# Kernel tuning notes

Measured on AMD Instinct MI355X. Metric: run time of the kernel, lower is better.

## Reference

```python
import jax, jax.numpy as jnp
import numpy as np

# ---- dimensions ----
N_MOL, N_PER = 256, 32
N = N_MOL * N_PER                      # 8192 nodes
E = N_MOL * N_PER * (N_PER - 1)        # 253952 fully-connected directed edges
SDIM, VDIM, EDIM = 256, 64, 32
NAF, NBT, LAT = 16, 5, 64
LAYERS = 5
MSG_IN = 2 * SDIM + EDIM + 2           # [s_i, s_j, e, d, a]
MSG_OUT = SDIM + VDIM + 1 + EDIM       # scalar msg, vec weights, pos weight, edge update
BOND_IN = SDIM + EDIM + 1
BOND_HID = 128


def _block_fc_edges():
    # fully-connected (no self loops) edges within each molecule of N_PER atoms
    idx = np.arange(N_PER)
    src, tgt = np.meshgrid(idx, idx, indexing='ij')
    mask = src != tgt
    src, tgt = src[mask], tgt[mask]
    offs = (np.arange(N_MOL) * N_PER)[:, None]
    S = (src[None, :] + offs).reshape(-1)
    T = (tgt[None, :] + offs).reshape(-1)
    return np.stack([S, T], 0).astype(np.int64)


def setup_inputs() -> dict:
    key = jax.random.key(0)
    ks = jax.random.split(key, 16)
    edge_index = jnp.asarray(_block_fc_edges())
    batch = jnp.asarray(np.repeat(np.arange(N_MOL), N_PER).astype(np.int64))
    return dict(
        x=jax.random.normal(ks[0], (N, NAF), jnp.float32),
        z=jax.random.normal(ks[1], (N, LAT), jnp.float32),
        rot=jax.random.normal(ks[2], (N_MOL, 3, 3), jnp.float32),
        edge_index_global=edge_index,
        edge_attr_global=jax.random.normal(ks[3], (E, NBT), jnp.float32),
        batch=batch,
        # atom/bond input mappings (DenseLayer == Linear)
        Wam=jax.random.normal(ks[4], (NAF + LAT, SDIM + 3), jnp.float32) * 0.05,
        bam=jnp.zeros((SDIM + 3,), jnp.float32),
        Wbm=jax.random.normal(ks[5], (NBT, EDIM), jnp.float32) * 0.3,
        bbm=jnp.zeros((EDIM,), jnp.float32),
        # stacked per-layer EQGAT message-MLP weights
        gW1=jax.random.normal(ks[6], (LAYERS, MSG_IN, SDIM), jnp.float32) * 0.03,
        gb1=jnp.zeros((LAYERS, SDIM), jnp.float32),
        gW2=jax.random.normal(ks[7], (LAYERS, SDIM, MSG_OUT), jnp.float32) * 0.05,
        gb2=jnp.zeros((LAYERS, MSG_OUT), jnp.float32),
        # prediction heads
        Wh1=jax.random.normal(ks[8], (SDIM, SDIM), jnp.float32) * 0.05,
        bh1=jnp.zeros((SDIM,), jnp.float32),
        Wh2=jax.random.normal(ks[9], (SDIM, NAF), jnp.float32) * 0.05,
        bh2=jnp.zeros((NAF,), jnp.float32),
        We1=jax.random.normal(ks[10], (BOND_IN, BOND_HID), jnp.float32) * 0.05,
        be1=jnp.zeros((BOND_HID,), jnp.float32),
        We2=jax.random.normal(ks[11], (BOND_HID, NBT), jnp.float32) * 0.05,
        be2=jnp.zeros((NBT,), jnp.float32),
    )


def _edge_attrs(pos, src, tgt):
    # faithful to Decoder.calculate_edge_attrs (sqrt=True)
    r = pos[tgt] - pos[src]                       # [E,3]
    a = jnp.sum(pos[tgt] * pos[src], -1)          # [E]
    d = jnp.sqrt(jnp.clip(jnp.sum(r * r, -1), 1e-6))
    r_norm = r / (1.0 + d)[:, None]
    return d, a, r_norm


def reference(x, z, rot, edge_index_global, edge_attr_global, batch,
              Wam, bam, Wbm, bbm, gW1, gb1, gW2, gb2,
              Wh1, bh1, Wh2, bh2, We1, be1, We2, be2):
    src, tgt = edge_index_global[0], edge_index_global[1]
    n = x.shape[0]
    # atom mapping + split into scalar feats and positions
    h = jnp.concatenate([x, z], -1) @ Wam + bam
    s, pos = h[:, :SDIM], h[:, SDIM:]
    # per-graph rotation of positions
    pos = jnp.einsum('bij,bj->bi', rot[batch], pos)
    # bond mapping
    e = edge_attr_global @ Wbm + bbm
    v = jnp.zeros((n, 3, VDIM), x.dtype)
    # segment-mean denominator (in-degree), fixed since edge_index is fixed
    cnt = jnp.clip(jax.ops.segment_sum(jnp.ones((src.shape[0],), x.dtype), tgt,
                                       num_segments=n), 1.0)

    def seg_mean(m):
        out = jax.ops.segment_sum(m, tgt, num_segments=n)
        return out / cnt.reshape((n,) + (1,) * (m.ndim - 1))

    def layer(carry, p):
        s, v, pos, e = carry
        W1, b1, W2, b2 = p
        d, a, r_norm = _edge_attrs(pos, src, tgt)   # recompute_edge_attributes=True
        feat = jnp.concatenate([s[src], s[tgt], e, d[:, None], a[:, None]], -1)
        hdn = jax.nn.silu(feat @ W1 + b1)
        m = hdn @ W2 + b2
        m_s = m[:, :SDIM]
        m_v = m[:, SDIM:SDIM + VDIM]
        m_p = m[:, SDIM + VDIM:SDIM + VDIM + 1]
        m_e = m[:, SDIM + VDIM + 1:]
        s = s + seg_mean(m_s)                                   # scalar update
        v = v + seg_mean(r_norm[:, :, None] * m_v[:, None, :])  # equivariant vec update
        pos = pos + seg_mean(r_norm * m_p)                      # equivariant pos update
        e = e + m_e                                             # edge feature update
        return (s, v, pos, e), None

    (s, v, pos, e), _ = jax.lax.scan(layer, (s, v, pos, e), (gW1, gb1, gW2, gb2))

    # prediction head: atom logits, bond logits (symmetric s_i+s_j), coords
    atoms = jax.nn.silu(s @ Wh1 + bh1) @ Wh2 + bh2
    d, a, r_norm = _edge_attrs(pos, src, tgt)
    ef = jnp.concatenate([s[src] + s[tgt], e, d[:, None]], -1)
    bonds = jax.nn.silu(ef @ We1 + be1) @ We2 + be2
    return atoms, bonds, pos
```

## Files before the change

kernel.cpp:

```cpp
#include <hip/hip_runtime.h>
#include <hip/hip_bf16.h>
#include <cstdint>
#include <cstddef>

#define N_MOLS 256
#define NN     8192
#define SDIM_  256
#define NAF_   16
#define LAYERS_ 5

typedef __attribute__((ext_vector_type(8)))  short bf16x8;
typedef __attribute__((ext_vector_type(16))) float f32x16;
typedef __attribute__((ext_vector_type(4)))  float f32x4;

__device__ __forceinline__ float silu_f(float x) {
    return x * __builtin_amdgcn_rcpf(1.f + __expf(-x));
}
__device__ __forceinline__ short bfc(float f) {
    __hip_bfloat16 h = __float2bfloat16(f);
    return __builtin_bit_cast(short, h);
}
__device__ __forceinline__ float bf2f(short h) {
    union { uint32_t u; float f; } v; v.u = ((uint32_t)(unsigned short)h) << 16; return v.f;
}
#define ONEBF ((short)0x3F80)

#define OFF_T1    0
#define OFF_W2ST  655360
#define OFF_WH1T  983040
#define OFF_WE1T  1048576
#define OFF_W1CG  1081344
#define OFF_W1DA  1122304
#define OFF_W2P   1124864
#define OFF_W2EI  1126144
#define OFF_WE1CG 1167104
#define OFF_WD    1171200
#define OFF_WE2I  1171328
#define OFF_WH2T  1175424
#define W_TOTAL   1179520

__global__ __launch_bounds__(256) void init_all(
    const float* __restrict__ x, const float* __restrict__ z,
    const float* __restrict__ rot, const float* __restrict__ Wam,
    const float* __restrict__ bam, const float* __restrict__ ea,
    const float* __restrict__ Wbm, const float* __restrict__ bbm,
    const float* __restrict__ gW1, const float* __restrict__ gW2,
    const float* __restrict__ Wh1, const float* __restrict__ We1,
    const float* __restrict__ We2, const float* __restrict__ Wh2,
    float* __restrict__ s, short* __restrict__ sbf, float* __restrict__ pos,
    short* __restrict__ ebuf, short* __restrict__ wb)
{
    __shared__ __align__(16) char smem[20608];
    const int b = blockIdx.x, t = threadIdx.x;
    if (b < 1024) {
        for (int o = b * 256 + t; o < W_TOTAL; o += 1024 * 256) {
            float v;
            if (o < OFF_W2ST) {
                const int l = o >> 17, r = o & 131071;
                const int j2 = r >> 8, k = r & 255;
                v = gW1[(size_t)l * 139776 + (size_t)((j2 >> 8) * 256 + k) * 256 + (j2 & 255)];
            } else if (o < OFF_WH1T) {
                const int q = o - OFF_W2ST;
                const int l = q >> 16, r = q & 65535;
                const int n = r >> 8, k = r & 255;
                v = gW2[(size_t)l * 90368 + (size_t)k * 353 + n];
            } else if (o < OFF_WE1T) {
                const int q = o - OFF_WH1T;
                v = Wh1[(size_t)(q & 255) * 256 + (q >> 8)];
            } else if (o < OFF_W1CG) {
                const int q = o - OFF_WE1T;
                v = We1[(size_t)(q & 255) * 128 + (q >> 8)];
            } else if (o < OFF_W1DA) {
                const int q = o - OFF_W1CG;
                const int l = q >> 13, r = q & 8191;
                const int j = r >> 5, w = r & 31;
                v = gW1[(size_t)l * 139776 + (size_t)(512 + w) * 256 + j];
            } else if (o < OFF_W2P) {
                const int q = o - OFF_W1DA;
                const int l = q >> 9, r = q & 511;
                v = gW1[(size_t)l * 139776 + (size_t)(544 + (r >> 8)) * 256 + (r & 255)];
            } else if (o < OFF_W2EI) {
                const int q = o - OFF_W2P;
                v = gW2[(size_t)(q >> 8) * 90368 + (size_t)(q & 255) * 353 + 320];
            } else if (o < OFF_WE1CG) {
                const int q = o - OFF_W2EI;
                const int l = q >> 13, r = q & 8191;
                const int kk = r >> 9, lanei = (r >> 3) & 63, jj = r & 7;
                const int j = kk * 16 + (lanei >> 5) * 8 + jj;
                v = gW2[(size_t)l * 90368 + (size_t)j * 353 + 321 + (lanei & 31)];
            } else if (o < OFF_WD) {
                const int q = o - OFF_WE1CG;
                v = We1[(size_t)(256 + (q & 31)) * 128 + (q >> 5)];
            } else if (o < OFF_WE2I) {
                v = We1[288 * 128 + (o - OFF_WD)];
            } else if (o < OFF_WH2T) {
                const int q = o - OFF_WE2I;
                const int kk = q >> 9, lanei = (q >> 3) & 63, jj = q & 7;
                const int c = lanei & 31;
                v = (c < 5) ? We2[(size_t)(kk * 16 + (lanei >> 5) * 8 + jj) * 5 + c] : 0.f;
            } else {
                const int q = o - OFF_WH2T;
                v = Wh2[(size_t)(q & 255) * 16 + (q >> 8)];
            }
            wb[o] = bfc(v);
        }
    } else if (b < 1280) {
        const int mol = b - 1024;
        float (*xz)[80]  = (float(*)[80])smem;
        float (*praw)[3] = (float(*)[3])(smem + 32 * 80 * 4);
        for (int idx = t; idx < 32 * 80; idx += 256) {
            const int i = idx / 80, k = idx % 80;
            xz[i][k] = (k < 16) ? x[(size_t)(mol * 32 + i) * 16 + k]
                                : z[(size_t)(mol * 32 + i) * 64 + (k - 16)];
        }
        __syncthreads();
        float acc[32];
        #pragma unroll
        for (int i = 0; i < 32; ++i) acc[i] = 0.f;
        for (int k0 = 0; k0 < 80; k0 += 4) {
            const float w0 = Wam[(k0 + 0) * 259 + t];
            const float w1 = Wam[(k0 + 1) * 259 + t];
            const float w2 = Wam[(k0 + 2) * 259 + t];
            const float w3 = Wam[(k0 + 3) * 259 + t];
            #pragma unroll
            for (int i = 0; i < 32; ++i) {
                const float4 xv = *(const float4*)&xz[i][k0];
                acc[i] += xv.x * w0 + xv.y * w1 + xv.z * w2 + xv.w * w3;
            }
        }
        const float bv = bam[t];
        #pragma unroll
        for (int i = 0; i < 32; ++i) {
            const float v = acc[i] + bv;
            s[(size_t)(mol * 32 + i) * 256 + t] = v;
            sbf[(size_t)(mol * 32 + i) * 256 + t] = bfc(v);
        }
        if (t < 96) {
            const int i = t / 3, c = t % 3;
            float a2 = bam[256 + c];
            for (int k = 0; k < 80; ++k) a2 += xz[i][k] * Wam[k * 259 + 256 + c];
            praw[i][c] = a2;
        }
        __syncthreads();
        if (t < 96) {
            const int i = t / 3, c = t % 3;
            float p = 0.f;
            for (int jj = 0; jj < 3; ++jj) p += rot[mol * 9 + c * 3 + jj] * praw[i][jj];
            pos[(size_t)(mol * 32 + i) * 3 + c] = p;
        }
    } else {
        const int mol = b - 1280;
        float* sEa      = (float*)smem;
        float (*sW)[32] = (float(*)[32])(smem + 4960 * 4);
        float* sB       = (float*)(smem + (4960 + 160) * 4);
        const float* base = ea + (size_t)mol * 4960;
        for (int i = t; i < 4960; i += 256) sEa[i] = base[i];
        if (t < 160) sW[t / 32][t & 31] = Wbm[t];
        if (t < 32)  sB[t] = bbm[t];
        __syncthreads();
        for (int i = t; i < 31744; i += 256) {
            const int c = i & 31;
            const int rrn = i >> 5;
            const int n = rrn / 31, rr = rrn - n * 31;
            const int s_ = rr + (rr >= n ? 1 : 0);
            const int gl = s_ * 31 + (n - (n > s_ ? 1 : 0));
            float acc = sB[c];
            #pragma unroll
            for (int k = 0; k < 5; ++k) acc += sEa[gl * 5 + k] * sW[k][c];
            ebuf[(size_t)mol * 31744 + i] = bfc(acc);
        }
    }
}

__global__ __launch_bounds__(512) void edge_mfma(
    const short* __restrict__ sbfA, const short* __restrict__ T1,
    const float* __restrict__ posIn, float* __restrict__ posOut,
    short* __restrict__ ebuf,
    const short* __restrict__ W1cG, const short* __restrict__ W1daP,
    const short* __restrict__ W2pP, const short* __restrict__ W2eimg,
    const short* __restrict__ W2sT,
    const float* __restrict__ b1, const float* __restrict__ b2,
    float* __restrict__ s, short* __restrict__ sbfOut)
{
    const int blk = blockIdx.x;
    const int mol = blk >> 1;
    const int nbase = (blk & 1) * 16;
    const int t = threadIdx.x;
    const int wave = t >> 6, lane = t & 63;
    const int l = lane & 31, half = lane >> 5;
    const int node0 = mol * 32;

    __shared__ __align__(16) short sBg[256][72];
    __shared__ __align__(16) short sM[8][32][40];
    __shared__ __align__(16) short sHrows[16][264];
    __shared__ __align__(16) short sSB[16][264];
    __shared__ float sPosS[32][4];
    __shared__ __align__(16) short sW1da[2][256];
    __shared__ __align__(16) short sW2p[256];
    __shared__ float sP[8][32];
    __shared__ float sPd[16][4];
    short* sSbf = &sM[0][0][0];

    {
        const int j = t & 255, gh = t >> 8;
        const bf16x8 v0 = *(const bf16x8*)&W1cG[j * 32 + gh * 16];
        const bf16x8 v1 = *(const bf16x8*)&W1cG[j * 32 + gh * 16 + 8];
        const int c3 = (j >> 3) & 3;
        const int s0 = ((gh * 2 + 0) + 3 * c3) & 7;
        const int s1 = ((gh * 2 + 1) + 3 * c3) & 7;
        *(bf16x8*)&sBg[j][s0 * 8] = v0;
        *(bf16x8*)&sBg[j][s1 * 8] = v1;
    }
    {
        const int row = t >> 4, ch = (t & 15) * 16;
        const short* src = sbfA + (size_t)(node0 + row) * 256 + ch;
        *(bf16x8*)&sSbf[row * 264 + ch]     = *(const bf16x8*)(src);
        *(bf16x8*)&sSbf[row * 264 + ch + 8] = *(const bf16x8*)(src + 8);
    }
    if (t < 64) {
        short* d = &sW1da[0][0];
        *(bf16x8*)&d[t * 8] = *(const bf16x8*)&W1daP[t * 8];
    }
    if (t < 32) *(bf16x8*)&sW2p[t * 8] = *(const bf16x8*)&W2pP[t * 8];
    if (t < 96) sPosS[t / 3][t % 3] = posIn[node0 * 3 + t];
    __syncthreads();

    {
        const int jt = wave;
        const int j = jt * 32 + l;
        f32x16 accA = {}, accB = {};
        #pragma unroll
        for (int k0 = 0; k0 < 256; k0 += 16) {
            const bf16x8 afr = *(const bf16x8*)&sSbf[l * 264 + k0 + half * 8];
            const bf16x8 bA  = *(const bf16x8*)(T1 + (size_t)(j) * 256 + k0 + half * 8);
            const bf16x8 bB  = *(const bf16x8*)(T1 + (size_t)(256 + j) * 256 + k0 + half * 8);
            accA = __builtin_amdgcn_mfma_f32_32x32x16_bf16(afr, bA, accA, 0,0,0);
            accB = __builtin_amdgcn_mfma_f32_32x32x16_bf16(afr, bB, accB, 0,0,0);
        }
        const int c3 = (j >> 3) & 3;
        #pragma unroll
        for (int r = 0; r < 16; ++r) {
            const int node = (r & 3) + 8 * (r >> 2) + 4 * half;
            const int k = 32 + node;
            const int slot = ((k >> 3) + 3 * c3) & 7;
            sBg[j][slot * 8 + (k & 7)] = bfc(accA[r]);
            const int nl = node - nbase;
            if ((unsigned)nl < 16u) sSB[nl][j] = bfc(accB[r]);
        }
    }
    __syncthreads();

    float b1v[8];
    short w1dv[8], w1av[8];
    #pragma unroll
    for (int cb = 0; cb < 8; ++cb) {
        b1v[cb]  = b1[cb * 32 + l];
        w1dv[cb] = sW1da[0][cb * 32 + l];
        w1av[cb] = sW1da[1][cb * 32 + l];
    }
    const float b2e = b2[321 + l];
    const float b2p = b2[320];
    int bslot[4];
    #pragma unroll
    for (int ks = 0; ks < 4; ++ks)
        bslot[ks] = ((ks * 2 + half) + 3 * ((l >> 3) & 3)) & 7;

    bf16x8 efr0[2], efr1[2];
    #pragma unroll
    for (int ni = 0; ni < 2; ++ni) {
        const int n = nbase + wave + ni * 8;
        const short* ebase = ebuf + ((size_t)((mol * 32 + n) * 31 + l)) * 32;
        efr0[ni] = *(const bf16x8*)(ebase + half * 8);
        efr1[ni] = *(const bf16x8*)(ebase + 16 + half * 8);
    }

    #pragma unroll
    for (int ni = 0; ni < 2; ++ni) {
        const int n = nbase + wave + ni * 8;
        const int nloc = wave + ni * 8;
        const int rrc = (l < 31) ? l : 30;
        const int src = rrc + (rrc >= n ? 1 : 0);
        const float ax = sPosS[n][0],  ay = sPosS[n][1],  az = sPosS[n][2];
        const float bx = sPosS[src][0], by = sPosS[src][1], bz = sPosS[src][2];
        const float rx = ax - bx, ry = ay - by, rz = az - bz;
        const float av = ax * bx + ay * by + az * bz;
        const float dd = sqrtf(fmaxf(rx * rx + ry * ry + rz * rz, 1e-6f));
        const float inv = __builtin_amdgcn_rcpf(1.f + dd);
        const float rnx = rx * inv, rny = ry * inv, rnz = rz * inv;

        const bf16x8 fr0 = efr0[ni];
        const bf16x8 fr1 = efr1[ni];
        bf16x8 fr2 = {}, fr3, fr4;
        if (half == 0) { fr2[0] = bfc(dd); fr2[1] = bfc(av); }
        #pragma unroll
        for (int jj = 0; jj < 8; ++jj) {
            fr3[jj] = (half * 8 + jj == src)      ? ONEBF : (short)0;
            fr4[jj] = (16 + half * 8 + jj == src) ? ONEBF : (short)0;
        }

        const short* W2ei = W2eimg;
        asm volatile("" : "+s"(W2ei));

        f32x16 accC = {}, accP = {};
        float Hacc[8];

        const int g = l >> 3, jlow = l & 7;
        #pragma unroll
        for (int cb = 0; cb < 8; ++cb) {
            const bf16x8 w2e0 = *(const bf16x8*)&W2ei[(size_t)((cb * 2 + 0) * 64 + lane) * 8];
            const bf16x8 w2e1 = *(const bf16x8*)&W2ei[(size_t)((cb * 2 + 1) * 64 + lane) * 8];
            const float sbv = bf2f(sSB[nloc][cb * 32 + l]) + b1v[cb];
            f32x16 acc;
            #pragma unroll
            for (int r = 0; r < 16; ++r) acc[r] = sbv;
            {
                const short* brow = &sBg[cb * 32 + l][0];
                __builtin_amdgcn_s_setprio(1);
                acc = __builtin_amdgcn_mfma_f32_32x32x16_bf16(fr0, *(const bf16x8*)(brow + bslot[0]*8), acc, 0,0,0);
                acc = __builtin_amdgcn_mfma_f32_32x32x16_bf16(fr1, *(const bf16x8*)(brow + bslot[1]*8), acc, 0,0,0);
                acc = __builtin_amdgcn_mfma_f32_32x32x16_bf16(fr3, *(const bf16x8*)(brow + bslot[2]*8), acc, 0,0,0);
                acc = __builtin_amdgcn_mfma_f32_32x32x16_bf16(fr4, *(const bf16x8*)(brow + bslot[3]*8), acc, 0,0,0);
                bf16x8 frB2 = {};
                if (half == 0) { frB2[0] = w1dv[cb]; frB2[1] = w1av[cb]; }
                acc = __builtin_amdgcn_mfma_f32_32x32x16_bf16(fr2, frB2, acc, 0,0,0);
                __builtin_amdgcn_s_setprio(0);
            }
            float hs = 0.f;
            #pragma unroll
            for (int r = 0; r < 16; ++r) {
                const int e = (r & 3) + 8 * (r >> 2) + 4 * half;
                float h = silu_f(acc[r]);
                if (half == 1 && r == 15) h = 0.f;
                hs += h;
                sM[wave][e][((g + (e >> 3)) & 3) * 8 + jlow] = bfc(h);
            }
            Hacc[cb] = hs;
            #pragma unroll
            for (int q = 0; q < 2; ++q) {
                const bf16x8 afr  = *(const bf16x8*)&sM[wave][l][((q * 2 + half + (l >> 3)) & 3) * 8];
                const bf16x8 wpfr = *(const bf16x8*)&sW2p[cb * 32 + q * 16 + half * 8];
                accC = __builtin_amdgcn_mfma_f32_32x32x16_bf16(afr, q ? w2e1 : w2e0, accC, 0,0,0);
                accP = __builtin_amdgcn_mfma_f32_32x32x16_bf16(afr, wpfr, accP, 0,0,0);
            }
        }
        #pragma unroll
        for (int cb = 0; cb < 8; ++cb) {
            const float v = Hacc[cb] + __shfl_xor(Hacc[cb], 32, 64);
            if (lane < 32) sHrows[nloc][cb * 32 + lane] = bfc(v);
        }
        if (l == 0) {
            #pragma unroll
            for (int q4 = 0; q4 < 4; ++q4) {
                float4 pv = { accP[q4 * 4 + 0], accP[q4 * 4 + 1],
                              accP[q4 * 4 + 2], accP[q4 * 4 + 3] };
                *(float4*)&sP[wave][q4 * 8 + 4 * half] = pv;
            }
        }
        const float pown = sP[wave][l];
        const float pfull = (half == 0 && l < 31) ? (pown + b2p) : 0.f;
        float pd0 = rnx * pfull, pd1 = rny * pfull, pd2 = rnz * pfull;
        #pragma unroll
        for (int m = 1; m <= 32; m <<= 1) {
            pd0 += __shfl_xor(pd0, m, 64);
            pd1 += __shfl_xor(pd1, m, 64);
            pd2 += __shfl_xor(pd2, m, 64);
        }
        if (lane == 0) {
            sPd[nloc][0] = pd0;
            sPd[nloc][1] = pd1;
            sPd[nloc][2] = pd2;
        }
        #pragma unroll
        for (int r = 0; r < 16; ++r) {
            const int e = (r & 3) + 8 * (r >> 2) + 4 * half;
            if (e < 31) {
                short* ep = ebuf + ((size_t)((mol * 32 + n) * 31 + e)) * 32 + l;
                *ep = bfc(bf2f(*ep) + accC[r] + b2e);
            }
        }
    }

    __syncthreads();

    {
        const int jb0 = wave * 32;
        const int arow = lane & 15, kg = lane >> 4;
        f32x4 accS0 = {}, accS1 = {};
        #pragma unroll
        for (int k0 = 0; k0 < 256; k0 += 32) {
            const bf16x8 afr = *(const bf16x8*)&sHrows[arow][k0 + kg * 8];
            const bf16x8 bf0 = *(const bf16x8*)&W2sT[(size_t)(jb0 + arow) * 256 + k0 + kg * 8];
            const bf16x8 bf1 = *(const bf16x8*)&W2sT[(size_t)(jb0 + 16 + arow) * 256 + k0 + kg * 8];
            accS0 = __builtin_amdgcn_mfma_f32_16x16x32_bf16(afr, bf0, accS0, 0,0,0);
            accS1 = __builtin_amdgcn_mfma_f32_16x16x32_bf16(afr, bf1, accS1, 0,0,0);
        }
        const int col = lane & 15;
        const int orow = (lane >> 4) * 4;
        const float bv0 = b2[jb0 + col];
        const float bv1 = b2[jb0 + 16 + col];
        #pragma unroll
        for (int r = 0; r < 4; ++r) {
            const int node = node0 + nbase + orow + r;
            {
                float* sp = s + (size_t)node * 256 + jb0 + col;
                const float nv = *sp + accS0[r] * (1.f / 31.f) + bv0;
                *sp = nv;
                sbfOut[(size_t)node * 256 + jb0 + col] = bfc(nv);
            }
            {
                float* sp = s + (size_t)node * 256 + jb0 + 16 + col;
                const float nv = *sp + accS1[r] * (1.f / 31.f) + bv1;
                *sp = nv;
                sbfOut[(size_t)node * 256 + jb0 + 16 + col] = bfc(nv);
            }
        }
    }
    if (t < 48) {
        const int nl = t / 3, c = t % 3;
        const int node = node0 + nbase + nl;
        posOut[(size_t)node * 3 + c] = posIn[(size_t)node * 3 + c] + sPd[nl][c] * (1.f / 31.f);
    }
}

__global__ __launch_bounds__(512) void bond_mfma(
    const short* __restrict__ sbfA, const short* __restrict__ We1T,
    const float* __restrict__ pos, short* __restrict__ ebuf,
    const short* __restrict__ We1cG, const short* __restrict__ WdP,
    const short* __restrict__ We2img, const short* __restrict__ Wh1T,
    const short* __restrict__ Wh2I,
    const float* __restrict__ be1, const float* __restrict__ be2,
    const float* __restrict__ bh1, const float* __restrict__ bh2,
    float* __restrict__ outA, float* __restrict__ outB,
    float* __restrict__ outPos)
{
    const int blk = blockIdx.x;
    const int mol = blk >> 1;
    const int nbase = (blk & 1) * 16;
    const int t = threadIdx.x;
    const int wave = t >> 6, lane = t & 63;
    const int l = lane & 31, half = lane >> 5;
    const int node0 = mol * 32;

    __shared__ __align__(16) short sBg2[128][72];
    __shared__ __align__(16) short sHdnB[8][32][40];
    __shared__ __align__(16) short sU[32][136];
    __shared__ float sPosS[32][4];
    __shared__ __align__(16) short sWd[128];
    short* sSbf = &sHdnB[0][0][0];

    {
        const int j = t & 127, g = t >> 7;
        const bf16x8 v = *(const bf16x8*)&We1cG[j * 32 + g * 8];
        const int slot = (g + 3 * ((j >> 3) & 3)) & 7;
        *(bf16x8*)&sBg2[j][slot * 8] = v;
    }
    {
        const int row = t >> 4, ch = (t & 15) * 16;
        const short* src = sbfA + (size_t)(node0 + row) * 256 + ch;
        *(bf16x8*)&sSbf[row * 264 + ch]     = *(const bf16x8*)(src);
        *(bf16x8*)&sSbf[row * 264 + ch + 8] = *(const bf16x8*)(src + 8);
    }
    if (t < 16) *(bf16x8*)&sWd[t * 8] = *(const bf16x8*)&WdP[t * 8];
    if (t < 96) sPosS[t / 3][t % 3] = pos[node0 * 3 + t];
    __syncthreads();

    if (wave < 4) {
        const int j = wave * 32 + l;
        f32x16 accU = {};
        #pragma unroll
        for (int k0 = 0; k0 < 256; k0 += 16) {
            const bf16x8 afr = *(const bf16x8*)&sSbf[l * 264 + k0 + half * 8];
            const bf16x8 bU  = *(const bf16x8*)(We1T + (size_t)j * 256 + k0 + half * 8);
            accU = __builtin_amdgcn_mfma_f32_32x32x16_bf16(afr, bU, accU, 0,0,0);
        }
        const int c3 = (j >> 3) & 3;
        #pragma unroll
        for (int r = 0; r < 16; ++r) {
            const int node = (r & 3) + 8 * (r >> 2) + 4 * half;
            const short uv = bfc(accU[r]);
            const int k = 32 + node;
            const int slot = ((k >> 3) + 3 * c3) & 7;
            sBg2[j][slot * 8 + (k & 7)] = uv;
            sU[node][j] = uv;
        }
    }

    float be1v[4];
    #pragma unroll
    for (int cb = 0; cb < 4; ++cb) be1v[cb] = be1[cb * 32 + l];
    const float be2v = (l < 5) ? be2[l] : 0.f;
    int bslot[4];
    #pragma unroll
    for (int ks = 0; ks < 4; ++ks)
        bslot[ks] = ((ks * 2 + half) + 3 * ((l >> 3) & 3)) & 7;
    __syncthreads();

    bf16x8 efr0[2], efr1[2];
    #pragma unroll
    for (int ni = 0; ni < 2; ++ni) {
        const int n = nbase + wave + ni * 8;
        const short* ebase = ebuf + ((size_t)((mol * 32 + n) * 31 + l)) * 32;
        efr0[ni] = *(const bf16x8*)(ebase + half * 8);
        efr1[ni] = *(const bf16x8*)(ebase + 16 + half * 8);
    }

    #pragma unroll
    for (int ni = 0; ni < 2; ++ni) {
        const int n = nbase + wave + ni * 8;
        const int rrc = (l < 31) ? l : 30;
        const int src = rrc + (rrc >= n ? 1 : 0);
        const float rx = sPosS[n][0] - sPosS[src][0];
        const float ry = sPosS[n][1] - sPosS[src][1];
        const float rz = sPosS[n][2] - sPosS[src][2];
        const float dd = sqrtf(fmaxf(rx * rx + ry * ry + rz * rz, 1e-6f));

        const bf16x8 fr0 = efr0[ni];
        const bf16x8 fr1 = efr1[ni];
        bf16x8 fr2 = {}, fr3, fr4;
        if (half == 0) fr2[0] = bfc(dd);
        #pragma unroll
        for (int jj = 0; jj < 8; ++jj) {
            fr3[jj] = (half * 8 + jj == src)      ? ONEBF : (short)0;
            fr4[jj] = (16 + half * 8 + jj == src) ? ONEBF : (short)0;
        }

        const short* We2i = We2img;
        asm volatile("" : "+s"(We2i));

        f32x16 accC = {};
        const int g = l >> 3, jlow = l & 7;
        #pragma unroll
        for (int cb = 0; cb < 4; ++cb) {
            const bf16x8 w2f0 = *(const bf16x8*)&We2i[(size_t)((cb * 2 + 0) * 64 + lane) * 8];
            const bf16x8 w2f1 = *(const bf16x8*)&We2i[(size_t)((cb * 2 + 1) * 64 + lane) * 8];
            const float uin = bf2f(sU[n][cb * 32 + l]) + be1v[cb];
            f32x16 acc;
            #pragma unroll
            for (int r = 0; r < 16; ++r) acc[r] = uin;
            {
                const short* brow = &sBg2[cb * 32 + l][0];
                acc = __builtin_amdgcn_mfma_f32_32x32x16_bf16(fr0, *(const bf16x8*)(brow + bslot[0]*8), acc, 0,0,0);
                acc = __builtin_amdgcn_mfma_f32_32x32x16_bf16(fr1, *(const bf16x8*)(brow + bslot[1]*8), acc, 0,0,0);
                acc = __builtin_amdgcn_mfma_f32_32x32x16_bf16(fr3, *(const bf16x8*)(brow + bslot[2]*8), acc, 0,0,0);
                acc = __builtin_amdgcn_mfma_f32_32x32x16_bf16(fr4, *(const bf16x8*)(brow + bslot[3]*8), acc, 0,0,0);
                bf16x8 frWd = {};
                if (half == 0) frWd[0] = sWd[cb * 32 + l];
                acc = __builtin_amdgcn_mfma_f32_32x32x16_bf16(fr2, frWd, acc, 0,0,0);
            }
            #pragma unroll
            for (int r = 0; r < 16; ++r) {
                const int e = (r & 3) + 8 * (r >> 2) + 4 * half;
                sHdnB[wave][e][((g + (e >> 3)) & 3) * 8 + jlow] = bfc(silu_f(acc[r]));
            }
            #pragma unroll
            for (int q = 0; q < 2; ++q) {
                const bf16x8 afr = *(const bf16x8*)&sHdnB[wave][l][((q * 2 + half + (l >> 3)) & 3) * 8];
                accC = __builtin_amdgcn_mfma_f32_32x32x16_bf16(afr, q ? w2f1 : w2f0, accC, 0,0,0);
            }
        }
        if (l < 5) {
            #pragma unroll
            for (int r = 0; r < 16; ++r) {
                const int e = (r & 3) + 8 * (r >> 2) + 4 * half;
                if (e < 31) {
                    const int s_ = e + (e >= n ? 1 : 0);
                    const int ge = (mol * 32 + s_) * 31 + (n - (n > s_ ? 1 : 0));
                    outB[(size_t)ge * 5 + l] = accC[r] + be2v;
                }
            }
        }
    }
    if (t < 48) {
        const int nl = t / 3, c = t % 3;
        const int node = node0 + nbase + nl;
        outPos[(size_t)node * 3 + c] = pos[(size_t)node * 3 + c];
    }

    __syncthreads();
    {
        short* sA3 = &sU[0][0];
        const int row = t >> 5, ch = (t & 31) * 8;
        *(bf16x8*)&sA3[row * 264 + ch] =
            *(const bf16x8*)(sbfA + (size_t)(node0 + nbase + row) * 256 + ch);
    }
    __syncthreads();
    {
        short* sA3 = &sU[0][0];
        short* sT  = &sBg2[0][0];
        const int jb0 = wave * 32;
        const int arow = lane & 15, kg = lane >> 4;
        f32x4 a0 = {}, a1 = {};
        #pragma unroll
        for (int k0 = 0; k0 < 256; k0 += 32) {
            const bf16x8 afr = *(const bf16x8*)&sA3[arow * 264 + k0 + kg * 8];
            const bf16x8 bw0 = *(const bf16x8*)(Wh1T + (size_t)(jb0 + arow) * 256 + k0 + kg * 8);
            const bf16x8 bw1 = *(const bf16x8*)(Wh1T + (size_t)(jb0 + 16 + arow) * 256 + k0 + kg * 8);
            a0 = __builtin_amdgcn_mfma_f32_16x16x32_bf16(afr, bw0, a0, 0,0,0);
            a1 = __builtin_amdgcn_mfma_f32_16x16x32_bf16(afr, bw1, a1, 0,0,0);
        }
        const int col = lane & 15, orow = (lane >> 4) * 4;
        const float bva = bh1[jb0 + col], bvb = bh1[jb0 + 16 + col];
        #pragma unroll
        for (int r = 0; r < 4; ++r) {
            sT[(orow + r) * 264 + jb0 + col]      = bfc(silu_f(a0[r] + bva));
            sT[(orow + r) * 264 + jb0 + 16 + col] = bfc(silu_f(a1[r] + bvb));
        }
    }
    __syncthreads();
    if (wave == 0) {
        short* sT = &sBg2[0][0];
        const int arow = lane & 15, kg = lane >> 4;
        f32x4 a2 = {};
        #pragma unroll
        for (int k0 = 0; k0 < 256; k0 += 32) {
            const bf16x8 afr = *(const bf16x8*)&sT[arow * 264 + k0 + kg * 8];
            const bf16x8 bfr = *(const bf16x8*)(Wh2I + (size_t)arow * 256 + k0 + kg * 8);
            a2 = __builtin_amdgcn_mfma_f32_16x16x32_bf16(afr, bfr, a2, 0,0,0);
        }
        const int col = lane & 15, orow = (lane >> 4) * 4;
        const float bv = bh2[col];
        #pragma unroll
        for (int r = 0; r < 4; ++r)
            outA[(size_t)(node0 + nbase + orow + r) * 16 + col] = a2[r] + bv;
    }
}

extern "C" void kernel_launch(void* const* d_in, const int* in_sizes, int n_in,
                              void* d_out, int out_size, void* d_ws, size_t ws_size,
                              hipStream_t stream) {
    const float* x   = (const float*)d_in[0];
    const float* z   = (const float*)d_in[1];
    const float* rot = (const float*)d_in[2];
    const float* ea  = (const float*)d_in[4];
    const float* Wam = (const float*)d_in[6];
    const float* bam = (const float*)d_in[7];
    const float* Wbm = (const float*)d_in[8];
    const float* bbm = (const float*)d_in[9];
    const float* gW1 = (const float*)d_in[10];
    const float* gb1 = (const float*)d_in[11];
    const float* gW2 = (const float*)d_in[12];
    const float* gb2 = (const float*)d_in[13];
    const float* Wh1 = (const float*)d_in[14];
    const float* bh1 = (const float*)d_in[15];
    const float* Wh2 = (const float*)d_in[16];
    const float* bh2 = (const float*)d_in[17];
    const float* We1 = (const float*)d_in[18];
    const float* be1 = (const float*)d_in[19];
    const float* We2 = (const float*)d_in[20];
    const float* be2 = (const float*)d_in[21];
    float* out = (float*)d_out;

    float* ws  = (float*)d_ws;
    float* s    = ws;
    float* pos  = ws + 2097152;
    short* e    = (short*)(ws + 2121728);
    short* wb   = (short*)(ws + 6184960);
    short* sbf0 = (short*)(ws + 6774784);
    short* sbf1 = (short*)(ws + 10248192);
    float* pos2 = ws + 16539648;

    init_all<<<1536, 256, 0, stream>>>(x, z, rot, Wam, bam, ea, Wbm, bbm,
        gW1, gW2, Wh1, We1, We2, Wh2, s, sbf0, pos, e, wb);

    float* pbuf[2] = { pos, pos2 };
    short* sbb[2] = { sbf0, sbf1 };
    for (int l = 0; l < LAYERS_; ++l) {
        const float* b1 = gb1 + l * 256;
        const float* b2 = gb2 + l * 353;
        edge_mfma<<<2 * N_MOLS, 512, 0, stream>>>(
            sbb[l & 1], wb + OFF_T1 + (size_t)l * 131072,
            pbuf[l & 1], pbuf[(l + 1) & 1], e,
            wb + OFF_W1CG + l * 8192, wb + OFF_W1DA + l * 512,
            wb + OFF_W2P + l * 256, wb + OFF_W2EI + l * 8192,
            wb + OFF_W2ST + (size_t)l * 65536,
            b1, b2, s, sbb[(l + 1) & 1]);
    }
    float* posF = pbuf[LAYERS_ & 1];
    short* sbfF = sbb[LAYERS_ & 1];

    bond_mfma<<<2 * N_MOLS, 512, 0, stream>>>(
        sbfF, wb + OFF_WE1T, posF, e, wb + OFF_WE1CG, wb + OFF_WD,
        wb + OFF_WE2I, wb + OFF_WH1T, wb + OFF_WH2T,
        be1, be2, bh1, bh2, out, out + 131072, out + 131072 + 1269760);
}
```

Measured before the change: 581.8 us.

## Fuse all five message-passing layers into one persistent per-molecule kernel

Replaces the five per-layer edge kernel launches (two blocks per molecule) with a single 1024-thread block per molecule that loops over layers. Node scalar bf16 features and positions stay in shared memory across layers, which removes the global round-trips, the ping-pong buffers and the launch gaps between layers. It also stops the duplicated T1 GEMM: previously each half-block recomputed both halves, now the 16 waves split the work. The cost is one block per molecule, so only 256 blocks, more shared memory per block and possibly lower occupancy.

```diff
diff --git a/kernel.cpp b/kernel.cpp
--- a/kernel.cpp
+++ b/kernel.cpp
@@ -172,253 +172,268 @@
     }
 }
 
-__global__ __launch_bounds__(512) void edge_mfma(
-    const short* __restrict__ sbfA, const short* __restrict__ T1,
-    const float* __restrict__ posIn, float* __restrict__ posOut,
-    short* __restrict__ ebuf,
-    const short* __restrict__ W1cG, const short* __restrict__ W1daP,
-    const short* __restrict__ W2pP, const short* __restrict__ W2eimg,
-    const short* __restrict__ W2sT,
-    const float* __restrict__ b1, const float* __restrict__ b2,
-    float* __restrict__ s, short* __restrict__ sbfOut)
+__global__ __launch_bounds__(1024) void mol_layers(
+    short* __restrict__ sbf_g, float* __restrict__ pos_g,
+    short* __restrict__ ebuf, const short* __restrict__ wb,
+    const float* __restrict__ gb1, const float* __restrict__ gb2,
+    float* __restrict__ s)
 {
-    const int blk = blockIdx.x;
-    const int mol = blk >> 1;
-    const int nbase = (blk & 1) * 16;
+    const int mol = blockIdx.x;
     const int t = threadIdx.x;
-    const int wave = t >> 6, lane = t & 63;
+    const int w = t >> 6, lane = t & 63;
     const int l = lane & 31, half = lane >> 5;
+    const int vw = w & 7, vb = w >> 3;
+    const int nbase = vb * 16;
     const int node0 = mol * 32;
 
     __shared__ __align__(16) short sBg[256][72];
-    __shared__ __align__(16) short sM[8][32][40];
-    __shared__ __align__(16) short sHrows[16][264];
-    __shared__ __align__(16) short sSB[16][264];
+    __shared__ __align__(16) short sM[16][32][40];
+    __shared__ __align__(16) short sHrows[32][264];
+    __shared__ __align__(16) short sSB[32][264];
+    __shared__ __align__(16) short sSbfP[32][264];
     __shared__ float sPosS[32][4];
     __shared__ __align__(16) short sW1da[2][256];
     __shared__ __align__(16) short sW2p[256];
-    __shared__ float sP[8][32];
-    __shared__ float sPd[16][4];
-    short* sSbf = &sM[0][0][0];
+    __shared__ float sP[16][32];
+    __shared__ float sPd[32][4];
 
     {
-        const int j = t & 255, gh = t >> 8;
-        const bf16x8 v0 = *(const bf16x8*)&W1cG[j * 32 + gh * 16];
-        const bf16x8 v1 = *(const bf16x8*)&W1cG[j * 32 + gh * 16 + 8];
-        const int c3 = (j >> 3) & 3;
-        const int s0 = ((gh * 2 + 0) + 3 * c3) & 7;
-        const int s1 = ((gh * 2 + 1) + 3 * c3) & 7;
-        *(bf16x8*)&sBg[j][s0 * 8] = v0;
-        *(bf16x8*)&sBg[j][s1 * 8] = v1;
-    }
-    {
-        const int row = t >> 4, ch = (t & 15) * 16;
-        const short* src = sbfA + (size_t)(node0 + row) * 256 + ch;
-        *(bf16x8*)&sSbf[row * 264 + ch]     = *(const bf16x8*)(src);
-        *(bf16x8*)&sSbf[row * 264 + ch + 8] = *(const bf16x8*)(src + 8);
-    }
-    if (t < 64) {
-        short* d = &sW1da[0][0];
-        *(bf16x8*)&d[t * 8] = *(const bf16x8*)&W1daP[t * 8];
-    }
-    if (t < 32) *(bf16x8*)&sW2p[t * 8] = *(const bf16x8*)&W2pP[t * 8];
-    if (t < 96) sPosS[t / 3][t % 3] = posIn[node0 * 3 + t];
-    __syncthreads();
-
-    {
-        const int jt = wave;
-        const int j = jt * 32 + l;
-        f32x16 accA = {}, accB = {};
-        #pragma unroll
-        for (int k0 = 0; k0 < 256; k0 += 16) {
-            const bf16x8 afr = *(const bf16x8*)&sSbf[l * 264 + k0 + half * 8];
-            const bf16x8 bA  = *(const bf16x8*)(T1 + (size_t)(j) * 256 + k0 + half * 8);
-            const bf16x8 bB  = *(const bf16x8*)(T1 + (size_t)(256 + j) * 256 + k0 + half * 8);
-            accA = __builtin_amdgcn_mfma_f32_32x32x16_bf16(afr, bA, accA, 0,0,0);
-            accB = __builtin_amdgcn_mfma_f32_32x32x16_bf16(afr, bB, accB, 0,0,0);
-        }
-        const int c3 = (j >> 3) & 3;
-        #pragma unroll
-        for (int r = 0; r < 16; ++r) {
-            const int node = (r & 3) + 8 * (r >> 2) + 4 * half;
-            const int k = 32 + node;
-            const int slot = ((k >> 3) + 3 * c3) & 7;
-            sBg[j][slot * 8 + (k & 7)] = bfc(accA[r]);
-            const int nl = node - nbase;
-            if ((unsigned)nl < 16u) sSB[nl][j] = bfc(accB[r]);
-        }
-    }
-    __syncthreads();
-
-    float b1v[8];
-    short w1dv[8], w1av[8];
-    #pragma unroll
-    for (int cb = 0; cb < 8; ++cb) {
-        b1v[cb]  = b1[cb * 32 + l];
-        w1dv[cb] = sW1da[0][cb * 32 + l];
-        w1av[cb] = sW1da[1][cb * 32 + l];
-    }
-    const float b2e = b2[321 + l];
-    const float b2p = b2[320];
+        const int row = t >> 5, ch = (t & 31) * 8;
+        *(bf16x8*)&sSbfP[row][ch] =
+            *(const bf16x8*)(sbf_g + (size_t)(node0 + row) * 256 + ch);
+    }
+    if (t < 96) sPosS[t / 3][t % 3] = pos_g[node0 * 3 + t];
+
     int bslot[4];
     #pragma unroll
     for (int ks = 0; ks < 4; ++ks)
         bslot[ks] = ((ks * 2 + half) + 3 * ((l >> 3) & 3)) & 7;
 
-    bf16x8 efr0[2], efr1[2];
-    #pragma unroll
-    for (int ni = 0; ni < 2; ++ni) {
-        const int n = nbase + wave + ni * 8;
-        const short* ebase = ebuf + ((size_t)((mol * 32 + n) * 31 + l)) * 32;
-        efr0[ni] = *(const bf16x8*)(ebase + half * 8);
-        efr1[ni] = *(const bf16x8*)(ebase + 16 + half * 8);
-    }
-
-    #pragma unroll
-    for (int ni = 0; ni < 2; ++ni) {
-        const int n = nbase + wave + ni * 8;
-        const int nloc = wave + ni * 8;
-        const int rrc = (l < 31) ? l : 30;
-        const int src = rrc + (rrc >= n ? 1 : 0);
-        const float ax = sPosS[n][0],  ay = sPosS[n][1],  az = sPosS[n][2];
-        const float bx = sPosS[src][0], by = sPosS[src][1], bz = sPosS[src][2];
-        const float rx = ax - bx, ry = ay - by, rz = az - bz;
-        const float av = ax * bx + ay * by + az * bz;
-        const float dd = sqrtf(fmaxf(rx * rx + ry * ry + rz * rz, 1e-6f));
-        const float inv = __builtin_amdgcn_rcpf(1.f + dd);
-        const float rnx = rx * inv, rny = ry * inv, rnz = rz * inv;
-
-        const bf16x8 fr0 = efr0[ni];
-        const bf16x8 fr1 = efr1[ni];
-        bf16x8 fr2 = {}, fr3, fr4;
-        if (half == 0) { fr2[0] = bfc(dd); fr2[1] = bfc(av); }
-        #pragma unroll
-        for (int jj = 0; jj < 8; ++jj) {
-            fr3[jj] = (half * 8 + jj == src)      ? ONEBF : (short)0;
-            fr4[jj] = (16 + half * 8 + jj == src) ? ONEBF : (short)0;
-        }
-
-        const short* W2ei = W2eimg;
-        asm volatile("" : "+s"(W2ei));
-
-        f32x16 accC = {}, accP = {};
-        float Hacc[8];
-
-        const int g = l >> 3, jlow = l & 7;
+    for (int ly = 0; ly < LAYERS_; ++ly) {
+        const short* T1     = wb + OFF_T1   + (size_t)ly * 131072;
+        const short* W1cG   = wb + OFF_W1CG + ly * 8192;
+        const short* W1daP  = wb + OFF_W1DA + ly * 512;
+        const short* W2pP   = wb + OFF_W2P  + ly * 256;
+        const short* W2eimg = wb + OFF_W2EI + ly * 8192;
+        const short* W2sT   = wb + OFF_W2ST + (size_t)ly * 65536;
+        const float* b1     = gb1 + ly * 256;
+        const float* b2     = gb2 + ly * 353;
+
+        __syncthreads();
+
+        {
+            const int j = t & 255, ks = t >> 8;
+            const bf16x8 v = *(const bf16x8*)&W1cG[j * 32 + ks * 8];
+            const int slot = (ks + 3 * ((j >> 3) & 3)) & 7;
+            *(bf16x8*)&sBg[j][slot * 8] = v;
+        }
+        if (t < 64) {
+            short* d = &sW1da[0][0];
+            *(bf16x8*)&d[t * 8] = *(const bf16x8*)&W1daP[t * 8];
+        }
+        if (t < 32) *(bf16x8*)&sW2p[t * 8] = *(const bf16x8*)&W2pP[t * 8];
+
+        {
+            const int j = vw * 32 + l;
+            const short* Bsrc = T1 + (size_t)(vb * 256 + j) * 256;
+            f32x16 acc = {};
+            #pragma unroll
+            for (int k0 = 0; k0 < 256; k0 += 16) {
+                const bf16x8 afr = *(const bf16x8*)&sSbfP[l][k0 + half * 8];
+                const bf16x8 bfr = *(const bf16x8*)(Bsrc + k0 + half * 8);
+                acc = __builtin_amdgcn_mfma_f32_32x32x16_bf16(afr, bfr, acc, 0,0,0);
+            }
+            const int c3 = (j >> 3) & 3;
+            if (vb == 0) {
+                #pragma unroll
+                for (int r = 0; r < 16; ++r) {
+                    const int node = (r & 3) + 8 * (r >> 2) + 4 * half;
+                    const int k = 32 + node;
+                    const int slot = ((k >> 3) + 3 * c3) & 7;
+                    sBg[j][slot * 8 + (k & 7)] = bfc(acc[r]);
+                }
+            } else {
+                #pragma unroll
+                for (int r = 0; r < 16; ++r) {
+                    const int node = (r & 3) + 8 * (r >> 2) + 4 * half;
+                    sSB[node][j] = bfc(acc[r]);
+                }
+            }
+        }
+        __syncthreads();
+
+        float b1v[8];
+        short w1dv[8], w1av[8];
         #pragma unroll
         for (int cb = 0; cb < 8; ++cb) {
-            const bf16x8 w2e0 = *(const bf16x8*)&W2ei[(size_t)((cb * 2 + 0) * 64 + lane) * 8];
-            const bf16x8 w2e1 = *(const bf16x8*)&W2ei[(size_t)((cb * 2 + 1) * 64 + lane) * 8];
-            const float sbv = bf2f(sSB[nloc][cb * 32 + l]) + b1v[cb];
-            f32x16 acc;
-            #pragma unroll
-            for (int r = 0; r < 16; ++r) acc[r] = sbv;
-            {
-                const short* brow = &sBg[cb * 32 + l][0];
-                __builtin_amdgcn_s_setprio(1);
-                acc = __builtin_amdgcn_mfma_f32_32x32x16_bf16(fr0, *(const bf16x8*)(brow + bslot[0]*8), acc, 0,0,0);
-                acc = __builtin_amdgcn_mfma_f32_32x32x16_bf16(fr1, *(const bf16x8*)(brow + bslot[1]*8), acc, 0,0,0);
-                acc = __builtin_amdgcn_mfma_f32_32x32x16_bf16(fr3, *(const bf16x8*)(brow + bslot[2]*8), acc, 0,0,0);
-                acc = __builtin_amdgcn_mfma_f32_32x32x16_bf16(fr4, *(const bf16x8*)(brow + bslot[3]*8), acc, 0,0,0);
-                bf16x8 frB2 = {};
-                if (half == 0) { frB2[0] = w1dv[cb]; frB2[1] = w1av[cb]; }
-                acc = __builtin_amdgcn_mfma_f32_32x32x16_bf16(fr2, frB2, acc, 0,0,0);
-                __builtin_amdgcn_s_setprio(0);
-            }
-            float hs = 0.f;
+            b1v[cb]  = b1[cb * 32 + l];
+            w1dv[cb] = sW1da[0][cb * 32 + l];
+            w1av[cb] = sW1da[1][cb * 32 + l];
+        }
+        const float b2e = b2[321 + l];
+        const float b2p = b2[320];
+
+        bf16x8 efr0[2], efr1[2];
+        #pragma unroll
+        for (int ni = 0; ni < 2; ++ni) {
+            const int n = nbase + vw + ni * 8;
+            const short* ebase = ebuf + ((size_t)((mol * 32 + n) * 31 + l)) * 32;
+            efr0[ni] = *(const bf16x8*)(ebase + half * 8);
+            efr1[ni] = *(const bf16x8*)(ebase + 16 + half * 8);
+        }
+
+        #pragma unroll
+        for (int ni = 0; ni < 2; ++ni) {
+            const int n = nbase + vw + ni * 8;
+            const int rrc = (l < 31) ? l : 30;
+            const int src = rrc + (rrc >= n ? 1 : 0);
+            const float ax = sPosS[n][0],  ay = sPosS[n][1],  az = sPosS[n][2];
+            const float bx = sPosS[src][0], by = sPosS[src][1], bz = sPosS[src][2];
+            const float rx = ax - bx, ry = ay - by, rz = az - bz;
+            const float av = ax * bx + ay * by + az * bz;
+            const float dd = sqrtf(fmaxf(rx * rx + ry * ry + rz * rz, 1e-6f));
+            const float inv = __builtin_amdgcn_rcpf(1.f + dd);
+            const float rnx = rx * inv, rny = ry * inv, rnz = rz * inv;
+
+            const bf16x8 fr0 = efr0[ni];
+            const bf16x8 fr1 = efr1[ni];
+            bf16x8 fr2 = {}, fr3, fr4;
+            if (half == 0) { fr2[0] = bfc(dd); fr2[1] = bfc(av); }
+            #pragma unroll
+            for (int jj = 0; jj < 8; ++jj) {
+                fr3[jj] = (half * 8 + jj == src)      ? ONEBF : (short)0;
+                fr4[jj] = (16 + half * 8 + jj == src) ? ONEBF : (short)0;
+            }
+
+            const short* W2ei = W2eimg;
+            asm volatile("" : "+s"(W2ei));
+
+            f32x16 accC = {}, accP = {};
+            float Hacc[8];
+
+            const int g = l >> 3, jlow = l & 7;
+            #pragma unroll
+            for (int cb = 0; cb < 8; ++cb) {
+                const bf16x8 w2e0 = *(const bf16x8*)&W2ei[(size_t)((cb * 2 + 0) * 64 + lane) * 8];
+                const bf16x8 w2e1 = *(const bf16x8*)&W2ei[(size_t)((cb * 2 + 1) * 64 + lane) * 8];
+                const float sbv = bf2f(sSB[n][cb * 32 + l]) + b1v[cb];
+                f32x16 acc;
+                #pragma unroll
+                for (int r = 0; r < 16; ++r) acc[r] = sbv;
+                {
+                    const short* brow = &sBg[cb * 32 + l][0];
+                    __builtin_amdgcn_s_setprio(1);
+                    acc = __builtin_amdgcn_mfma_f32_32x32x16_bf16(fr0, *(const bf16x8*)(brow + bslot[0]*8), acc, 0,0,0);
+                    acc = __builtin_amdgcn_mfma_f32_32x32x16_bf16(fr1, *(const bf16x8*)(brow + bslot[1]*8), acc, 0,0,0);
+                    acc = __builtin_amdgcn_mfma_f32_32x32x16_bf16(fr3, *(const bf16x8*)(brow + bslot[2]*8), acc, 0,0,0);
+                    acc = __builtin_amdgcn_mfma_f32_32x32x16_bf16(fr4, *(const bf16x8*)(brow + bslot[3]*8), acc, 0,0,0);
+                    bf16x8 frB2 = {};
+                    if (half == 0) { frB2[0] = w1dv[cb]; frB2[1] = w1av[cb]; }
+                    acc = __builtin_amdgcn_mfma_f32_32x32x16_bf16(fr2, frB2, acc, 0,0,0);
+                    __builtin_amdgcn_s_setprio(0);
+                }
+                float hs = 0.f;
+                #pragma unroll
+                for (int r = 0; r < 16; ++r) {
+                    const int e = (r & 3) + 8 * (r >> 2) + 4 * half;
+                    float h = silu_f(acc[r]);
+                    if (half == 1 && r == 15) h = 0.f;
+                    hs += h;
+                    sM[w][e][((g + (e >> 3)) & 3) * 8 + jlow] = bfc(h);
+                }
+                Hacc[cb] = hs;
+                #pragma unroll
+                for (int q = 0; q < 2; ++q) {
+                    const bf16x8 afr  = *(const bf16x8*)&sM[w][l][((q * 2 + half + (l >> 3)) & 3) * 8];
+                    const bf16x8 wpfr = *(const bf16x8*)&sW2p[cb * 32 + q * 16 + half * 8];
+                    accC = __builtin_amdgcn_mfma_f32_32x32x16_bf16(afr, q ? w2e1 : w2e0, accC, 0,0,0);
+                    accP = __builtin_amdgcn_mfma_f32_32x32x16_bf16(afr, wpfr, accP, 0,0,0);
+                }
+            }
+            #pragma unroll
+            for (int cb = 0; cb < 8; ++cb) {
+                const float v = Hacc[cb] + __shfl_xor(Hacc[cb], 32, 64);
+                if (lane < 32) sHrows[n][cb * 32 + lane] = bfc(v);
+            }
+            if (l == 0) {
+                #pragma unroll
+                for (int q4 = 0; q4 < 4; ++q4) {
+                    float4 pv = { accP[q4 * 4 + 0], accP[q4 * 4 + 1],
+                                  accP[q4 * 4 + 2], accP[q4 * 4 + 3] };
+                    *(float4*)&sP[w][q4 * 8 + 4 * half] = pv;
+                }
+            }
+            const float pown = sP[w][l];
+            const float pfull = (half == 0 && l < 31) ? (pown + b2p) : 0.f;
+            float pd0 = rnx * pfull, pd1 = rny * pfull, pd2 = rnz * pfull;
+            #pragma unroll
+            for (int m = 1; m <= 32; m <<= 1) {
+                pd0 += __shfl_xor(pd0, m, 64);
+                pd1 += __shfl_xor(pd1, m, 64);
+                pd2 += __shfl_xor(pd2, m, 64);
+            }
+            if (lane == 0) {
+                sPd[n][0] = pd0;
+                sPd[n][1] = pd1;
+                sPd[n][2] = pd2;
+            }
             #pragma unroll
             for (int r = 0; r < 16; ++r) {
                 const int e = (r & 3) + 8 * (r >> 2) + 4 * half;
-                float h = silu_f(acc[r]);
-                if (half == 1 && r == 15) h = 0.f;
-                hs += h;
-                sM[wave][e][((g + (e >> 3)) & 3) * 8 + jlow] = bfc(h);
-            }
-            Hacc[cb] = hs;
-            #pragma unroll
-            for (int q = 0; q < 2; ++q) {
-                const bf16x8 afr  = *(const bf16x8*)&sM[wave][l][((q * 2 + half + (l >> 3)) & 3) * 8];
-                const bf16x8 wpfr = *(const bf16x8*)&sW2p[cb * 32 + q * 16 + half * 8];
-                accC = __builtin_amdgcn_mfma_f32_32x32x16_bf16(afr, q ? w2e1 : w2e0, accC, 0,0,0);
-                accP = __builtin_amdgcn_mfma_f32_32x32x16_bf16(afr, wpfr, accP, 0,0,0);
-            }
-        }
-        #pragma unroll
-        for (int cb = 0; cb < 8; ++cb) {
-            const float v = Hacc[cb] + __shfl_xor(Hacc[cb], 32, 64);
-            if (lane < 32) sHrows[nloc][cb * 32 + lane] = bfc(v);
-        }
-        if (l == 0) {
-            #pragma unroll
-            for (int q4 = 0; q4 < 4; ++q4) {
-                float4 pv = { accP[q4 * 4 + 0], accP[q4 * 4 + 1],
-                              accP[q4 * 4 + 2], accP[q4 * 4 + 3] };
-                *(float4*)&sP[wave][q4 * 8 + 4 * half] = pv;
-            }
-        }
-        const float pown = sP[wave][l];
-        const float pfull = (half == 0 && l < 31) ? (pown + b2p) : 0.f;
-        float pd0 = rnx * pfull, pd1 = rny * pfull, pd2 = rnz * pfull;
-        #pragma unroll
-        for (int m = 1; m <= 32; m <<= 1) {
-            pd0 += __shfl_xor(pd0, m, 64);
-            pd1 += __shfl_xor(pd1, m, 64);
-            pd2 += __shfl_xor(pd2, m, 64);
-        }
-        if (lane == 0) {
-            sPd[nloc][0] = pd0;
-            sPd[nloc][1] = pd1;
-            sPd[nloc][2] = pd2;
-        }
-        #pragma unroll
-        for (int r = 0; r < 16; ++r) {
-            const int e = (r & 3) + 8 * (r >> 2) + 4 * half;
-            if (e < 31) {
-                short* ep = ebuf + ((size_t)((mol * 32 + n) * 31 + e)) * 32 + l;
-                *ep = bfc(bf2f(*ep) + accC[r] + b2e);
-            }
-        }
-    }
-
-    __syncthreads();
-
-    {
-        const int jb0 = wave * 32;
-        const int arow = lane & 15, kg = lane >> 4;
-        f32x4 accS0 = {}, accS1 = {};
-        #pragma unroll
-        for (int k0 = 0; k0 < 256; k0 += 32) {
-            const bf16x8 afr = *(const bf16x8*)&sHrows[arow][k0 + kg * 8];
-            const bf16x8 bf0 = *(const bf16x8*)&W2sT[(size_t)(jb0 + arow) * 256 + k0 + kg * 8];
-            const bf16x8 bf1 = *(const bf16x8*)&W2sT[(size_t)(jb0 + 16 + arow) * 256 + k0 + kg * 8];
-            accS0 = __builtin_amdgcn_mfma_f32_16x16x32_bf16(afr, bf0, accS0, 0,0,0);
-            accS1 = __builtin_amdgcn_mfma_f32_16x16x32_bf16(afr, bf1, accS1, 0,0,0);
-        }
-        const int col = lane & 15;
-        const int orow = (lane >> 4) * 4;
-        const float bv0 = b2[jb0 + col];
-        const float bv1 = b2[jb0 + 16 + col];
-        #pragma unroll
-        for (int r = 0; r < 4; ++r) {
-            const int node = node0 + nbase + orow + r;
-            {
-                float* sp = s + (size_t)node * 256 + jb0 + col;
-                const float nv = *sp + accS0[r] * (1.f / 31.f) + bv0;
-                *sp = nv;
-                sbfOut[(size_t)node * 256 + jb0 + col] = bfc(nv);
-            }
-            {
-                float* sp = s + (size_t)node * 256 + jb0 + 16 + col;
-                const float nv = *sp + accS1[r] * (1.f / 31.f) + bv1;
-                *sp = nv;
-                sbfOut[(size_t)node * 256 + jb0 + 16 + col] = bfc(nv);
-            }
-        }
-    }
-    if (t < 48) {
-        const int nl = t / 3, c = t % 3;
-        const int node = node0 + nbase + nl;
-        posOut[(size_t)node * 3 + c] = posIn[(size_t)node * 3 + c] + sPd[nl][c] * (1.f / 31.f);
+                if (e < 31) {
+                    short* ep = ebuf + ((size_t)((mol * 32 + n) * 31 + e)) * 32 + l;
+                    *ep = bfc(bf2f(*ep) + accC[r] + b2e);
+                }
+            }
+        }
+
+        __syncthreads();
+
+        {
+            const int jb0 = vw * 32;
+            const int arow = lane & 15, kg = lane >> 4;
+            const int lrow = nbase + arow;
+            f32x4 accS0 = {}, accS1 = {};
+            #pragma unroll
+            for (int k0 = 0; k0 < 256; k0 += 32) {
+                const bf16x8 afr = *(const bf16x8*)&sHrows[lrow][k0 + kg * 8];
+                const bf16x8 bf0 = *(const bf16x8*)&W2sT[(size_t)(jb0 + arow) * 256 + k0 + kg * 8];
+                const bf16x8 bf1 = *(const bf16x8*)&W2sT[(size_t)(jb0 + 16 + arow) * 256 + k0 + kg * 8];
+                accS0 = __builtin_amdgcn_mfma_f32_16x16x32_bf16(afr, bf0, accS0, 0,0,0);
+                accS1 = __builtin_amdgcn_mfma_f32_16x16x32_bf16(afr, bf1, accS1, 0,0,0);
+            }
+            const int col = lane & 15;
+            const int orow = (lane >> 4) * 4;
+            const float bv0 = b2[jb0 + col];
+            const float bv1 = b2[jb0 + 16 + col];
+            #pragma unroll
+            for (int r = 0; r < 4; ++r) {
+                const int nl = nbase + orow + r;
+                const int node = node0 + nl;
+                {
+                    float* sp = s + (size_t)node * 256 + jb0 + col;
+                    const float nv = *sp + accS0[r] * (1.f / 31.f) + bv0;
+                    *sp = nv;
+                    const short bv = bfc(nv);
+                    sSbfP[nl][jb0 + col] = bv;
+                    if (ly == LAYERS_ - 1) sbf_g[(size_t)node * 256 + jb0 + col] = bv;
+                }
+                {
+                    float* sp = s + (size_t)node * 256 + jb0 + 16 + col;
+                    const float nv = *sp + accS1[r] * (1.f / 31.f) + bv1;
+                    *sp = nv;
+                    const short bv = bfc(nv);
+                    sSbfP[nl][jb0 + 16 + col] = bv;
+                    if (ly == LAYERS_ - 1) sbf_g[(size_t)node * 256 + jb0 + 16 + col] = bv;
+                }
+            }
+        }
+        if (t < 96) {
+            const int nl = t / 3, c = t % 3;
+            const float np = sPosS[nl][c] + sPd[nl][c] * (1.f / 31.f);
+            sPosS[nl][c] = np;
+            if (ly == LAYERS_ - 1) pos_g[(size_t)(node0 + nl) * 3 + c] = np;
+        }
     }
 }
 
@@ -656,30 +671,14 @@
     short* e    = (short*)(ws + 2121728);
     short* wb   = (short*)(ws + 6184960);
     short* sbf0 = (short*)(ws + 6774784);
-    short* sbf1 = (short*)(ws + 10248192);
-    float* pos2 = ws + 16539648;
 
     init_all<<<1536, 256, 0, stream>>>(x, z, rot, Wam, bam, ea, Wbm, bbm,
         gW1, gW2, Wh1, We1, We2, Wh2, s, sbf0, pos, e, wb);
 
-    float* pbuf[2] = { pos, pos2 };
-    short* sbb[2] = { sbf0, sbf1 };
-    for (int l = 0; l < LAYERS_; ++l) {
-        const float* b1 = gb1 + l * 256;
-        const float* b2 = gb2 + l * 353;
-        edge_mfma<<<2 * N_MOLS, 512, 0, stream>>>(
-            sbb[l & 1], wb + OFF_T1 + (size_t)l * 131072,
-            pbuf[l & 1], pbuf[(l + 1) & 1], e,
-            wb + OFF_W1CG + l * 8192, wb + OFF_W1DA + l * 512,
-            wb + OFF_W2P + l * 256, wb + OFF_W2EI + l * 8192,
-            wb + OFF_W2ST + (size_t)l * 65536,
-            b1, b2, s, sbb[(l + 1) & 1]);
-    }
-    float* posF = pbuf[LAYERS_ & 1];
-    short* sbfF = sbb[LAYERS_ & 1];
+    mol_layers<<<N_MOLS, 1024, 0, stream>>>(sbf0, pos, e, wb, gb1, gb2, s);
 
     bond_mfma<<<2 * N_MOLS, 512, 0, stream>>>(
-        sbfF, wb + OFF_WE1T, posF, e, wb + OFF_WE1CG, wb + OFF_WD,
+        sbf0, wb + OFF_WE1T, pos, e, wb + OFF_WE1CG, wb + OFF_WD,
         wb + OFF_WE2I, wb + OFF_WH1T, wb + OFF_WH2T,
         be1, be2, bh1, bh2, out, out + 131072, out + 131072 + 1269760);
 }
```

Result: slower. 1.283 ms (+120.5%).
